# Optimization experiments

Hardware: AMD Instinct MI355X
Metric: run time of the kernel (lower is better)

The kernel has to match this reference:

```python
import jax, jax.numpy as jnp
import numpy as np

SEQ = 8192
DIM = 1280
NHEADS = 16
HEAD_DIM = DIM // NHEADS  # 80
NSEG = 8
SEG = SEQ // NSEG  # 1024


def setup_inputs() -> dict:
    key = jax.random.key(0)
    ks = jax.random.split(key, 7)
    hidden_states = jax.random.normal(ks[0], (SEQ, DIM), jnp.float32)
    # realistic rotary embeddings: cos/sin of random angles, shape [S, head_dim]
    ang = jax.random.uniform(ks[1], (SEQ, HEAD_DIM), jnp.float32, 0.0, 2.0 * np.pi)
    cos = jnp.cos(ang)
    sin = jnp.sin(ang)
    qkv_w = jax.random.normal(ks[2], (3 * DIM, DIM), jnp.float32) * (DIM ** -0.5)
    qkv_b = jax.random.normal(ks[3], (3 * DIM,), jnp.float32) * 0.02
    proj_w = jax.random.normal(ks[4], (DIM, DIM), jnp.float32) * (DIM ** -0.5)
    proj_b = jax.random.normal(ks[5], (DIM,), jnp.float32) * 0.02
    cu_seqlens = jnp.arange(NSEG + 1, dtype=jnp.int32) * SEG  # equal segments
    return {"hidden_states": hidden_states, "cos": cos, "sin": sin,
            "qkv_w": qkv_w, "qkv_b": qkv_b, "proj_w": proj_w, "proj_b": proj_b,
            "cu_seqlens": cu_seqlens}


def _rope(x, cos, sin):
    # x: [S, H, D]; cos/sin: [S, D] broadcast over heads. Computed in fp32.
    x = x.astype(jnp.float32)
    d = x.shape[-1]
    x1, x2 = x[..., : d // 2], x[..., d // 2:]
    rot = jnp.concatenate([-x2, x1], axis=-1)
    return x * cos[:, None, :] + rot * sin[:, None, :]


def reference(hidden_states, cos, sin, qkv_w, qkv_b, proj_w, proj_b, cu_seqlens):
    S, dim = hidden_states.shape
    nseg = cu_seqlens.shape[0] - 1
    seg = S // nseg  # segments are equal-length; block-diagonal attention batches over them
    H, D = NHEADS, dim // NHEADS

    qkv = hidden_states @ qkv_w.T + qkv_b                 # [S, 3*dim]
    qkv = qkv.reshape(S, 3, H, D)
    q, k, v = qkv[:, 0], qkv[:, 1], qkv[:, 2]             # [S, H, D]

    in_dtype = hidden_states.dtype
    q = _rope(q, cos, sin).astype(in_dtype)
    k = _rope(k, cos, sin).astype(in_dtype)

    scale = D ** -0.5
    qs = q.reshape(nseg, seg, H, D)
    ks = k.reshape(nseg, seg, H, D)
    vs = v.reshape(nseg, seg, H, D)

    scores = jnp.einsum('bqhd,bkhd->bhqk', qs, ks) * scale  # [nseg, H, seg, seg]
    probs = jax.nn.softmax(scores, axis=-1)
    out = jnp.einsum('bhqk,bkhd->bqhd', probs, vs)          # [nseg, seg, H, D]
    out = out.reshape(S, H * D)
    return out @ proj_w.T + proj_b
```

## Files before the change

### kernel.cpp

```cpp
#include <hip/hip_runtime.h>

#define SEQ 8192
#define DIM 1280
#define NHEADS 16
#define HD 80
#define HDP 96
#define NSEG 8
#define SEG 1024
#define KVB 64
#define NSTEP (SEG / KVB)
#define PST 72

typedef float f32x4 __attribute__((ext_vector_type(4)));
typedef short bf16x8 __attribute__((ext_vector_type(8)));
typedef unsigned int u32;

__device__ __forceinline__ float fast_exp2(float x) {
  return __builtin_amdgcn_exp2f(x);
}

__device__ __forceinline__ short f2bf(float f) {
  unsigned int u = __builtin_bit_cast(unsigned int, f);
  u = (u + 0x7fff + ((u >> 16) & 1)) >> 16;
  return (short)u;
}

__device__ __forceinline__ float bf2f(short s) {
  u32 u = ((u32)(unsigned short)s) << 16;
  return __builtin_bit_cast(float, u);
}

__device__ __forceinline__ u32 cvt_pk_bf16(float lo, float hi) {
  u32 r;
  asm("v_cvt_pk_bf16_f32 %0, %1, %2" : "=v"(r) : "v"(lo), "v"(hi));
  return r;
}

typedef __attribute__((address_space(1))) const unsigned int glds_src_t;
typedef __attribute__((address_space(3))) unsigned int glds_dst_t;
__device__ __forceinline__ void gload_lds16(const void* g, void* l) {
  __builtin_amdgcn_global_load_lds((glds_src_t*)g, (glds_dst_t*)l, 16, 0, 0);
}

__global__ void cast_f32_bf16(const float* __restrict__ in, short* __restrict__ out, int n) {
  int n4 = n >> 2;
  for (int i = blockIdx.x * blockDim.x + threadIdx.x; i < n4; i += gridDim.x * blockDim.x) {
    float4 v = ((const float4*)in)[i];
    short4 o;
    o.x = f2bf(v.x); o.y = f2bf(v.y); o.z = f2bf(v.z); o.w = f2bf(v.w);
    ((short4*)out)[i] = o;
  }
}

__global__ __launch_bounds__(256) void gemm_bt_bias(
    const short* __restrict__ A, const short* __restrict__ B,
    const float* __restrict__ bias, float* __restrict__ C,
    short* __restrict__ Cb, int M, int N, int K) {
  __shared__ short As[2][128 * 64];
  __shared__ short Bs[2][128 * 64];
  int tid = threadIdx.x;
  int w = tid >> 6, l = tid & 63;
  int lrow = l & 15, lg = l >> 4;
  int bid = blockIdx.x;
  int cpx = gridDim.x >> 3;
  int lid = (bid & 7) * cpx + (bid >> 3);
  int ntx = N >> 7;
  int m0 = (lid / ntx) * 128, n0 = (lid % ntx) * 128;
  int wm = w & 1, wn = w >> 1;

  f32x4 acc[4][4] = {};

  const char* Abase = (const char*)A + (size_t)m0 * K * 2;
  const char* Bbase = (const char*)B + (size_t)n0 * K * 2;

#define STAGE_G(BUF, K0)                                                       \
  {                                                                            \
    _Pragma("unroll") for (int j = 0; j < 4; j++) {                            \
      int c = j * 256 + tid;                                                   \
      int row = c >> 3;                                                        \
      int slc = (c & 7) ^ (row & 7);                                           \
      size_t goff = (size_t)row * K * 2 + (size_t)(K0) * 2 + slc * 16;         \
      int loff = (j * 256 + w * 64) * 16;                                      \
      gload_lds16(Abase + goff, (char*)&As[BUF][0] + loff);                    \
      gload_lds16(Bbase + goff, (char*)&Bs[BUF][0] + loff);                    \
    }                                                                          \
  }

  STAGE_G(0, 0);
  asm volatile("s_waitcnt vmcnt(0)" ::: "memory");
  __builtin_amdgcn_s_barrier();
  asm volatile("" ::: "memory");

  for (int k0 = 0; k0 < K; k0 += 64) {
    int cur = (k0 >> 6) & 1;
    if (k0 + 64 < K) {
      STAGE_G(cur ^ 1, k0 + 64);
      asm volatile("s_waitcnt vmcnt(8)" ::: "memory");
    } else {
      asm volatile("s_waitcnt vmcnt(0)" ::: "memory");
    }
    __builtin_amdgcn_s_barrier();
    asm volatile("" ::: "memory");
#pragma unroll
    for (int kk = 0; kk < 2; kk++) {
      bf16x8 a[4], b[4];
#pragma unroll
      for (int mt = 0; mt < 4; mt++) {
        int row = wm * 64 + mt * 16 + lrow;
        int p = (kk * 4 + lg) ^ (row & 7);
        a[mt] = *(const bf16x8*)&As[cur][row * 64 + p * 8];
      }
#pragma unroll
      for (int nt = 0; nt < 4; nt++) {
        int row = wn * 64 + nt * 16 + lrow;
        int p = (kk * 4 + lg) ^ (row & 7);
        b[nt] = *(const bf16x8*)&Bs[cur][row * 64 + p * 8];
      }
#pragma unroll
      for (int mt = 0; mt < 4; mt++)
#pragma unroll
        for (int nt = 0; nt < 4; nt++)
          acc[mt][nt] = __builtin_amdgcn_mfma_f32_16x16x32_bf16(a[mt], b[nt], acc[mt][nt], 0, 0, 0);
    }
    __builtin_amdgcn_s_barrier();
    asm volatile("" ::: "memory");
  }

#pragma unroll
  for (int nt = 0; nt < 4; nt++) {
    int col = n0 + wn * 64 + nt * 16 + lrow;
    float bv = bias[col];
#pragma unroll
    for (int mt = 0; mt < 4; mt++) {
      int mrow = m0 + wm * 64 + mt * 16 + lg * 4;
      if (Cb) {
#pragma unroll
        for (int r = 0; r < 4; r++)
          Cb[(size_t)(mrow + r) * N + col] = f2bf(acc[mt][nt][r] + bv);
      } else {
#pragma unroll
        for (int r = 0; r < 4; r++)
          C[(size_t)(mrow + r) * N + col] = acc[mt][nt][r] + bv;
      }
    }
  }
}

__global__ void rope_qk(const short* __restrict__ qkv, const float* __restrict__ cosb,
                        const float* __restrict__ sinb, short* __restrict__ qg,
                        short* __restrict__ kg) {
  int t = blockIdx.x * blockDim.x + threadIdx.x;
  if (t >= SEQ * NHEADS * 40) return;
  int d = t % 40;
  int h = (t / 40) & 15;
  int s = t / 640;
  const short* row = qkv + (size_t)s * (3 * DIM);
  float c0 = cosb[s * HD + d], c1 = cosb[s * HD + d + 40];
  float s0 = sinb[s * HD + d], s1 = sinb[s * HD + d + 40];
  float x1 = bf2f(row[h * HD + d]), x2 = bf2f(row[h * HD + d + 40]);
  float q0 = x1 * c0 - x2 * s0;
  float q1 = x2 * c1 + x1 * s1;
  float y1 = bf2f(row[DIM + h * HD + d]), y2 = bf2f(row[DIM + h * HD + d + 40]);
  float k0 = y1 * c0 - y2 * s0;
  float k1 = y2 * c1 + y1 * s1;
  const float sc = 0.11180339887498949f * 1.4426950408889634f;
  size_t base = ((size_t)h * SEQ + s) * HDP;
  qg[base + d] = f2bf(q0 * sc);
  qg[base + d + 40] = f2bf(q1 * sc);
  kg[base + d] = f2bf(k0);
  kg[base + d + 40] = f2bf(k1);
  if (d < 16) { qg[base + 80 + d] = 0; kg[base + 80 + d] = 0; }
}

__global__ void v_transpose(const short* __restrict__ qkv, short* __restrict__ vt) {
  __shared__ short T[16][72];
  int st = blockIdx.x, dt = blockIdx.y, h = blockIdx.z;
  int d0 = dt * 16, s0 = st * 64;
  int t = threadIdx.x;
  int dd = t & 15, ss = t >> 4;
#pragma unroll
  for (int j = 0; j < 4; j++) {
    int s = ss + j * 16;
    T[dd][s] = qkv[(size_t)(s0 + s) * (3 * DIM) + 2 * DIM + h * HD + d0 + dd];
  }
  __syncthreads();
  int s2 = t & 63, dr = t >> 6;
#pragma unroll
  for (int j = 0; j < 4; j++) {
    int d = dr + j * 4;
    vt[((size_t)(h * HD + d0 + d)) * SEQ + s0 + s2] = T[d][s2];
  }
}

__global__ __launch_bounds__(512, 2) void attn_kernel(
    const short* __restrict__ qg, const short* __restrict__ kg,
    const short* __restrict__ vt, short* __restrict__ out) {
  __shared__ short Ks[2][64 * 128];
  __shared__ short Pl[8][32 * PST];
  int bid = blockIdx.x;
  int b = bid & 7, h = (bid >> 3) & 15, qt = bid >> 7;
  int tid = threadIdx.x;
  int w = tid >> 6, l = tid & 63;
  int lrow = l & 15, lg = l >> 4;
  int qbase_s = b * SEG + qt * 256 + w * 32;

  const short* qh = qg + (size_t)h * SEQ * HDP;
  const short* kh = kg + (size_t)h * SEQ * HDP;
  const short* vh = vt + (size_t)h * HD * SEQ;

#define STAGE_K(BUF, KEY0N)                                                    \
  {                                                                            \
    _Pragma("unroll") for (int sr = 0; sr < 2; sr++) {                         \
      int sbase = sr * 512 + w * 64;                                           \
      int ss = sbase + l;                                                      \
      int skey = ss >> 4, sc = ss & 15;                                        \
      int slc = sc ^ (skey & 7);                                               \
      const short* ssrc =                                                      \
          kh + (size_t)((KEY0N) + skey) * HDP + (slc < 12 ? slc * 8 : 0);      \
      gload_lds16(ssrc, (char*)&Ks[BUF][0] + sbase * 16);                      \
    }                                                                          \
  }

  bf16x8 qf[2][3];
#pragma unroll
  for (int mt = 0; mt < 2; mt++)
#pragma unroll
    for (int ks = 0; ks < 3; ks++)
      qf[mt][ks] = *(const bf16x8*)&qh[(size_t)(qbase_s + mt * 16 + lrow) * HDP + ks * 32 + lg * 8];

  f32x4 o[2][5] = {};
  float m_st[2] = {-1e30f, -1e30f};
  float l_st[2] = {0.f, 0.f};

  short* Pw = &Pl[w][0];

  STAGE_K(0, b * SEG);
  __syncthreads();

  for (int i = 0; i < NSTEP; i++) {
    int cur = i & 1;
    int key0 = b * SEG + i * KVB;
    if (i + 1 < NSTEP) {
      STAGE_K(cur ^ 1, key0 + KVB);
    }

    f32x4 sv[2][4] = {};
    __builtin_amdgcn_s_setprio(1);
#pragma unroll
    for (int kt = 0; kt < 4; kt++) {
      bf16x8 kf[3];
      int key = kt * 16 + lrow;
#pragma unroll
      for (int ks = 0; ks < 3; ks++) {
        int p = (ks * 4 + lg) ^ (key & 7);
        kf[ks] = *(const bf16x8*)&Ks[cur][key * 128 + p * 8];
      }
#pragma unroll
      for (int mt = 0; mt < 2; mt++)
#pragma unroll
        for (int ks = 0; ks < 3; ks++)
          sv[mt][kt] = __builtin_amdgcn_mfma_f32_16x16x32_bf16(kf[ks], qf[mt][ks], sv[mt][kt], 0, 0, 0);
    }
    __builtin_amdgcn_s_setprio(0);

    bf16x8 vf[5][2];
#pragma unroll
    for (int nt = 0; nt < 5; nt++)
#pragma unroll
      for (int ks = 0; ks < 2; ks++)
        vf[nt][ks] = *(const bf16x8*)&vh[(size_t)(nt * 16 + lrow) * SEQ + key0 + ks * 32 + lg * 8];

    float cm[2];
#pragma unroll
    for (int mt = 0; mt < 2; mt++) {
      float a0 = fmaxf(fmaxf(sv[mt][0][0], sv[mt][0][1]), fmaxf(sv[mt][0][2], sv[mt][0][3]));
      float a1 = fmaxf(fmaxf(sv[mt][1][0], sv[mt][1][1]), fmaxf(sv[mt][1][2], sv[mt][1][3]));
      float a2 = fmaxf(fmaxf(sv[mt][2][0], sv[mt][2][1]), fmaxf(sv[mt][2][2], sv[mt][2][3]));
      float a3 = fmaxf(fmaxf(sv[mt][3][0], sv[mt][3][1]), fmaxf(sv[mt][3][2], sv[mt][3][3]));
      float c = fmaxf(fmaxf(a0, a1), fmaxf(a2, a3));
      c = fmaxf(c, __shfl_xor(c, 16));
      c = fmaxf(c, __shfl_xor(c, 32));
      cm[mt] = c;
    }
    if (__any((cm[0] > m_st[0] + 8.f) || (cm[1] > m_st[1] + 8.f))) {
#pragma unroll
      for (int mt = 0; mt < 2; mt++) {
        float mn = fmaxf(m_st[mt], cm[mt]);
        float c = fast_exp2(m_st[mt] - mn);
        m_st[mt] = mn;
        l_st[mt] *= c;
        float cr[4];
#pragma unroll
        for (int r = 0; r < 4; r++) cr[r] = __shfl(c, lg * 4 + r);
#pragma unroll
        for (int nt = 0; nt < 5; nt++)
#pragma unroll
          for (int r = 0; r < 4; r++) o[mt][nt][r] *= cr[r];
      }
    }
#pragma unroll
    for (int mt = 0; mt < 2; mt++) {
      float rs = 0.f;
#pragma unroll
      for (int kt = 0; kt < 4; kt++) {
#pragma unroll
        for (int r = 0; r < 4; r++) {
          sv[mt][kt][r] = fast_exp2(sv[mt][kt][r] - m_st[mt]);
          rs += sv[mt][kt][r];
        }
        uint2 pk;
        pk.x = cvt_pk_bf16(sv[mt][kt][0], sv[mt][kt][1]);
        pk.y = cvt_pk_bf16(sv[mt][kt][2], sv[mt][kt][3]);
        *(uint2*)&Pw[(mt * 16 + lrow) * PST + kt * 16 + lg * 4] = pk;
      }
      rs += __shfl_xor(rs, 16);
      rs += __shfl_xor(rs, 32);
      l_st[mt] += rs;
    }

    bf16x8 pa[2][2];
#pragma unroll
    for (int mt = 0; mt < 2; mt++)
#pragma unroll
      for (int ks = 0; ks < 2; ks++)
        pa[mt][ks] = *(const bf16x8*)&Pw[(mt * 16 + lrow) * PST + ks * 32 + lg * 8];
    __builtin_amdgcn_s_setprio(1);
#pragma unroll
    for (int nt = 0; nt < 5; nt++)
#pragma unroll
      for (int mt = 0; mt < 2; mt++)
#pragma unroll
        for (int ks = 0; ks < 2; ks++)
          o[mt][nt] = __builtin_amdgcn_mfma_f32_16x16x32_bf16(pa[mt][ks], vf[nt][ks], o[mt][nt], 0, 0, 0);
    __builtin_amdgcn_s_setprio(0);

    __syncthreads();
  }

#pragma unroll
  for (int mt = 0; mt < 2; mt++) {
    float rl = 1.f / l_st[mt];
    float ir[4];
#pragma unroll
    for (int r = 0; r < 4; r++) ir[r] = __shfl(rl, lg * 4 + r);
#pragma unroll
    for (int r = 0; r < 4; r++) {
      int srow = qbase_s + mt * 16 + lg * 4 + r;
#pragma unroll
      for (int nt = 0; nt < 5; nt++)
        out[(size_t)srow * DIM + h * HD + nt * 16 + lrow] = f2bf(o[mt][nt][r] * ir[r]);
    }
  }
}

extern "C" void kernel_launch(void* const* d_in, const int* in_sizes, int n_in,
                              void* d_out, int out_size, void* d_ws, size_t ws_size,
                              hipStream_t stream) {
  const float* hidden = (const float*)d_in[0];
  const float* cosb = (const float*)d_in[1];
  const float* sinb = (const float*)d_in[2];
  const float* qkv_w = (const float*)d_in[3];
  const float* qkv_b = (const float*)d_in[4];
  const float* proj_w = (const float*)d_in[5];
  const float* proj_b = (const float*)d_in[6];

  char* ws = (char*)d_ws;
  short* qkv_bf = (short*)(ws);
  short* attn_o = (short*)(ws);
  short* wp_bf = (short*)(ws + 23068672);
  short* q_bf = (short*)(ws + 125829120);
  short* k_bf = (short*)(ws + 150994944);
  short* v_tb = (short*)(ws + 176160768);
  short* h_bf = (short*)(ws + 197132288);
  short* wq_bf = (short*)(ws + 218103808);

  cast_f32_bf16<<<4096, 256, 0, stream>>>(hidden, h_bf, SEQ * DIM);
  cast_f32_bf16<<<4096, 256, 0, stream>>>(qkv_w, wq_bf, 3 * DIM * DIM);
  gemm_bt_bias<<<1920, 256, 0, stream>>>(h_bf, wq_bf, qkv_b, nullptr, qkv_bf, SEQ, 3 * DIM, DIM);
  rope_qk<<<20480, 256, 0, stream>>>(qkv_bf, cosb, sinb, q_bf, k_bf);
  v_transpose<<<dim3(128, 5, 16), 256, 0, stream>>>(qkv_bf, v_tb);
  cast_f32_bf16<<<2048, 256, 0, stream>>>(proj_w, wp_bf, DIM * DIM);
  attn_kernel<<<512, 512, 0, stream>>>(q_bf, k_bf, v_tb, attn_o);
  gemm_bt_bias<<<640, 256, 0, stream>>>(attn_o, wp_bf, proj_b, (float*)d_out, nullptr, SEQ, DIM, DIM);
}
```

Measured before the change: 316.2 us.

## Use 256x256-tile 8-wave GEMM with phased prefetch for QKV projection

Adds a new GEMM kernel that computes 256x256 output tiles with 512 threads (8 waves, each covering 128x64), double-buffered LDS staged via global_load_lds in halves, and a four-phase schedule that interleaves the next tile's prefetch with MFMA blocks under barriers and raised priority. The QKV projection now launches 480 of these blocks instead of 1920 128x128 blocks. The aim is more operand reuse per LDS load and better overlap of global loads with matrix math. The cost is far fewer blocks (fewer than two waves of work across the CUs), more barriers per K-step, and higher register pressure from 128 accumulators per lane.

```diff
diff --git a/kernel.cpp b/kernel.cpp
--- a/kernel.cpp
+++ b/kernel.cpp
@@ -50,6 +50,131 @@
     o.x = f2bf(v.x); o.y = f2bf(v.y); o.z = f2bf(v.z); o.w = f2bf(v.w);
     ((short4*)out)[i] = o;
   }
+}
+
+__global__ __launch_bounds__(512, 1) void gemm256(
+    const short* __restrict__ A, const short* __restrict__ B,
+    const float* __restrict__ bias, float* __restrict__ C,
+    short* __restrict__ Cb, int M, int N, int K) {
+  __shared__ short As[2][16384];
+  __shared__ short Bs[2][16384];
+  int tid = threadIdx.x;
+  int w = tid >> 6, l = tid & 63;
+  int lrow = l & 15, lg = l >> 4;
+  int wm = w >> 2, wn = w & 3;
+  int bid = blockIdx.x;
+  int cpx = gridDim.x >> 3;
+  int lid = (bid & 7) * cpx + (bid >> 3);
+  int ntx = N >> 8;
+  int m0 = (lid / ntx) * 256, n0 = (lid % ntx) * 256;
+
+  const short* Ablk = A + (size_t)m0 * K;
+  const short* Bblk = B + (size_t)n0 * K;
+
+  f32x4 acc[8][4] = {};
+
+#define STG_HALF(LDSB, GBASE, HALF, K0)                                       \
+  {                                                                           \
+    _Pragma("unroll") for (int rr = 0; rr < 2; rr++) {                        \
+      int sb = rr * 512 + w * 64;                                             \
+      int ss2 = sb + l;                                                       \
+      int rl = ss2 >> 3, cc = ss2 & 7;                                        \
+      int sl = cc ^ (rl & 7);                                                 \
+      const short* sp = (GBASE) + (size_t)((HALF)*128 + rl) * K + (K0) + sl * 8; \
+      gload_lds16(sp, (char*)(LDSB) + (HALF)*16384 + sb * 16);                \
+    }                                                                         \
+  }
+
+#define LDA(MH, KS)                                                           \
+  _Pragma("unroll") for (int mt = 0; mt < 4; mt++) {                          \
+    int rowa = wm * 128 + ((MH)*4 + mt) * 16 + lrow;                          \
+    int pa_ = ((KS)*4 + lg) ^ (rowa & 7);                                     \
+    a[mt] = *(const bf16x8*)&As[cur][rowa * 64 + pa_ * 8];                    \
+  }
+#define LDB(KS)                                                               \
+  _Pragma("unroll") for (int nt = 0; nt < 4; nt++) {                          \
+    int rowb = wn * 64 + nt * 16 + lrow;                                      \
+    int pb_ = ((KS)*4 + lg) ^ (rowb & 7);                                     \
+    b[nt] = *(const bf16x8*)&Bs[cur][rowb * 64 + pb_ * 8];                    \
+  }
+#define MFMA16(MH)                                                            \
+  _Pragma("unroll") for (int mt = 0; mt < 4; mt++)                            \
+      _Pragma("unroll") for (int nt = 0; nt < 4; nt++)                        \
+          acc[(MH)*4 + mt][nt] = __builtin_amdgcn_mfma_f32_16x16x32_bf16(     \
+              a[mt], b[nt], acc[(MH)*4 + mt][nt], 0, 0, 0);
+#define PHASE_SYNC()                                                          \
+  __builtin_amdgcn_s_barrier();                                               \
+  asm volatile("s_waitcnt lgkmcnt(0)" ::: "memory");                          \
+  __builtin_amdgcn_sched_barrier(0);
+#define PHASE_END()                                                           \
+  __builtin_amdgcn_s_barrier();                                               \
+  asm volatile("" ::: "memory");
+
+  {
+    short* Ad = &As[0][0];
+    short* Bd = &Bs[0][0];
+    STG_HALF(Ad, Ablk, 0, 0);
+    STG_HALF(Ad, Ablk, 1, 0);
+    STG_HALF(Bd, Bblk, 0, 0);
+    STG_HALF(Bd, Bblk, 1, 0);
+  }
+  asm volatile("s_waitcnt vmcnt(0)" ::: "memory");
+  __builtin_amdgcn_s_barrier();
+  asm volatile("" ::: "memory");
+
+  int NT = K >> 6;
+  for (int t = 0; t < NT; ++t) {
+    int cur = t & 1;
+    int k1 = (t + 1) << 6;
+    bool pre = (t + 1 < NT);
+    short* Ad = &As[cur ^ 1][0];
+    short* Bd = &Bs[cur ^ 1][0];
+    bf16x8 a[4], b[4];
+    LDA(0, 0); LDB(0);
+    if (pre) { STG_HALF(Ad, Ablk, 0, k1); STG_HALF(Bd, Bblk, 0, k1); }
+    PHASE_SYNC();
+    __builtin_amdgcn_s_setprio(1); MFMA16(0); __builtin_amdgcn_s_setprio(0);
+    PHASE_END();
+    LDA(1, 0);
+    if (pre) { STG_HALF(Ad, Ablk, 1, k1); STG_HALF(Bd, Bblk, 1, k1); }
+    PHASE_SYNC();
+    __builtin_amdgcn_s_setprio(1); MFMA16(1); __builtin_amdgcn_s_setprio(0);
+    PHASE_END();
+    LDA(0, 1); LDB(1);
+    PHASE_SYNC();
+    __builtin_amdgcn_s_setprio(1); MFMA16(0); __builtin_amdgcn_s_setprio(0);
+    PHASE_END();
+    LDA(1, 1);
+    PHASE_SYNC();
+    __builtin_amdgcn_s_setprio(1); MFMA16(1); __builtin_amdgcn_s_setprio(0);
+    asm volatile("s_waitcnt vmcnt(0)" ::: "memory");
+    PHASE_END();
+  }
+
+#pragma unroll
+  for (int nt = 0; nt < 4; nt++) {
+    int col = n0 + wn * 64 + nt * 16 + lrow;
+    float bv = bias[col];
+#pragma unroll
+    for (int mt = 0; mt < 8; mt++) {
+      int mrow = m0 + wm * 128 + mt * 16 + lg * 4;
+      if (Cb) {
+#pragma unroll
+        for (int r = 0; r < 4; r++)
+          Cb[(size_t)(mrow + r) * N + col] = f2bf(acc[mt][nt][r] + bv);
+      } else {
+#pragma unroll
+        for (int r = 0; r < 4; r++)
+          C[(size_t)(mrow + r) * N + col] = acc[mt][nt][r] + bv;
+      }
+    }
+  }
+#undef STG_HALF
+#undef LDA
+#undef LDB
+#undef MFMA16
+#undef PHASE_SYNC
+#undef PHASE_END
 }
 
 __global__ __launch_bounds__(256) void gemm_bt_bias(
@@ -376,7 +501,7 @@
 
   cast_f32_bf16<<<4096, 256, 0, stream>>>(hidden, h_bf, SEQ * DIM);
   cast_f32_bf16<<<4096, 256, 0, stream>>>(qkv_w, wq_bf, 3 * DIM * DIM);
-  gemm_bt_bias<<<1920, 256, 0, stream>>>(h_bf, wq_bf, qkv_b, nullptr, qkv_bf, SEQ, 3 * DIM, DIM);
+  gemm256<<<480, 512, 0, stream>>>(h_bf, wq_bf, qkv_b, nullptr, qkv_bf, SEQ, 3 * DIM, DIM);
   rope_qk<<<20480, 256, 0, stream>>>(qkv_bf, cosb, sinb, q_bf, k_bf);
   v_transpose<<<dim3(128, 5, 16), 256, 0, stream>>>(qkv_bf, v_tb);
   cast_f32_bf16<<<2048, 256, 0, stream>>>(proj_w, wp_bf, DIM * DIM);
```

Measured after the change: 317.1 us. Within noise of the previous version (+0.3%).
